# Kernel tuning notes

Hardware: AMD Instinct MI355X
Metric: run time of the kernel (lower is better)

Reference implementation:

```python
import jax, jax.numpy as jnp
import numpy as np

N, E, H, C, G = 30000, 960000, 2, 128, 64
EPS = 1e-5

def _bn(x, g, b):
    m = x.mean(0)
    v = x.var(0)  # biased, as torch BN training
    return (x - m) * jax.lax.rsqrt(v + EPS) * g + b

def setup_inputs() -> dict:
    key = jax.random.key(0)
    ks = jax.random.split(key, 16)
    s = lambda fan: 1.0 / np.sqrt(fan)
    return {
        "x": jax.random.normal(ks[0], (N, 448), jnp.float32),
        "gat_w": jax.random.normal(ks[1], (448, H * C), jnp.float32) * s(448),
        "gat_a_src": jax.random.normal(ks[2], (H, C), jnp.float32) * s(C),
        "gat_a_dst": jax.random.normal(ks[3], (H, C), jnp.float32) * s(C),
        "gat_bias": jnp.zeros((H * C,), jnp.float32),
        "mlp_w": jax.random.normal(ks[4], (H * C, 128), jnp.float32) * s(H * C),
        "mlp_b": jnp.zeros((128,), jnp.float32),
        "bn0_g": jnp.ones((128,), jnp.float32), "bn0_b": jnp.zeros((128,), jnp.float32),
        "fc1_w": jax.random.normal(ks[5], (128, 512), jnp.float32) * s(128),
        "fc1_b": jnp.zeros((512,), jnp.float32),
        "bn1_g": jnp.ones((512,), jnp.float32), "bn1_b": jnp.zeros((512,), jnp.float32),
        "fc2_w": jax.random.normal(ks[6], (512, 256), jnp.float32) * s(512),
        "fc2_b": jnp.zeros((256,), jnp.float32),
        "bn2_g": jnp.ones((256,), jnp.float32), "bn2_b": jnp.zeros((256,), jnp.float32),
        "fc3_w": jax.random.normal(ks[7], (256, 1), jnp.float32) * s(256),
        "fc3_b": jnp.zeros((1,), jnp.float32),
        "bn3_g": jnp.ones((1,), jnp.float32), "bn3_b": jnp.zeros((1,), jnp.float32),
        "edge_index": jax.random.randint(ks[8], (2, E), 0, N, jnp.int32),
        "batch": jnp.sort(jax.random.randint(ks[9], (N,), 0, G, jnp.int32)),
    }

def reference(x, gat_w, gat_a_src, gat_a_dst, gat_bias, mlp_w, mlp_b,
              bn0_g, bn0_b, fc1_w, fc1_b, bn1_g, bn1_b, fc2_w, fc2_b,
              bn2_g, bn2_b, fc3_w, fc3_b, bn3_g, bn3_b, edge_index, batch):
    # --- GATConv (eval-mode dropout = identity), self-loops added per PyG default ---
    xp = (x @ gat_w).reshape(N, H, C)                       # [N,H,C]
    a_s = (xp * gat_a_src).sum(-1)                          # [N,H]
    a_d = (xp * gat_a_dst).sum(-1)                          # [N,H]
    loops = jnp.arange(N, dtype=edge_index.dtype)
    src = jnp.concatenate([edge_index[0], loops])
    dst = jnp.concatenate([edge_index[1], loops])
    e = jax.nn.leaky_relu(a_s[src] + a_d[dst], 0.2)         # [E+N,H]
    m = jax.ops.segment_max(e, dst, num_segments=N)
    e = jnp.exp(e - m[dst])
    denom = jax.ops.segment_sum(e, dst, num_segments=N)
    alpha = e / denom[dst]                                  # softmax over in-edges
    out = jax.ops.segment_sum(alpha[:, :, None] * xp[src], dst, num_segments=N)
    out = out.reshape(N, H * C) + gat_bias                  # [N, H*C]
    # --- Scatter mlp: ELU -> (Dropout id) -> Linear -> BN ---
    h = _bn(jax.nn.elu(out) @ mlp_w + mlp_b, bn0_g, bn0_b)  # [N,128]
    # --- global_add_pool ---
    hp = jax.ops.segment_sum(h, batch, num_segments=G)      # [G,128]
    # --- fc stack: (Linear,BN,ReLU,Dropout) x2, then Linear+BN ---
    z = jax.nn.relu(_bn(hp @ fc1_w + fc1_b, bn1_g, bn1_b))
    z = jax.nn.relu(_bn(z @ fc2_w + fc2_b, bn2_g, bn2_b))
    z = _bn(z @ fc3_w + fc3_b, bn3_g, bn3_b)
    return z.reshape(-1)  # num_classes == 1
```

## Files before the change

kernel.cpp:

```cpp
#include <hip/hip_runtime.h>

#define N_NODES 30000
#define N_EDGES 960000
#define NGRAPH  64
#define BN_EPS  1e-5f
#define NBUCKET 118
#define BCAP    10240
#define GC_STRIDE 16

typedef __bf16 bf16x8 __attribute__((ext_vector_type(8)));
typedef float  f32x4  __attribute__((ext_vector_type(4)));

__device__ __forceinline__ unsigned short f2bf(float f) {
  union { float f; unsigned u; } v; v.f = f;
  unsigned r = (v.u + 0x7FFFu + ((v.u >> 16) & 1u)) >> 16;
  return (unsigned short)r;
}
__device__ __forceinline__ float bf2f(unsigned short u) {
  union { unsigned u; float f; } v; v.u = ((unsigned)u) << 16;
  return v.f;
}
__device__ __forceinline__ float bflo(unsigned w) {
  union { unsigned u; float f; } v; v.u = w << 16; return v.f;
}
__device__ __forceinline__ float bfhi(unsigned w) {
  union { unsigned u; float f; } v; v.u = w & 0xFFFF0000u; return v.f;
}
__device__ __forceinline__ void gld_lds16(const void* g, void* l) {
  __builtin_amdgcn_global_load_lds(
      (const __attribute__((address_space(1))) unsigned int*)g,
      (__attribute__((address_space(3))) unsigned int*)l, 16, 0, 0);
}

__global__ void prep_kernel(const int* __restrict__ ei,
                            int2* __restrict__ binbuf, int* __restrict__ gcur,
                            const float* __restrict__ gw, const float* __restrict__ mw,
                            unsigned short* __restrict__ wth,
                            unsigned short* __restrict__ mwth, unsigned short* __restrict__ mwtl,
                            const int* __restrict__ batch, int* __restrict__ cnt) {
  int b = blockIdx.x;
  int tid = threadIdx.x;
  if (b < 938) {
    __shared__ int lcnt[NBUCKET], lbase[NBUCKET], lcur[NBUCKET];
    int i = b * 1024 + tid * 4;
    bool val = i < N_EDGES;
    int4 dv = {0, 0, 0, 0}, sv = {0, 0, 0, 0};
    if (val) {
      dv = *(const int4*)(ei + N_EDGES + i);
      sv = *(const int4*)(ei + i);
    }
    if (tid < NBUCKET) lcnt[tid] = 0;
    __syncthreads();
    int bk0 = dv.x >> 8, bk1 = dv.y >> 8, bk2 = dv.z >> 8, bk3 = dv.w >> 8;
    if (val) {
      atomicAdd(&lcnt[bk0], 1); atomicAdd(&lcnt[bk1], 1);
      atomicAdd(&lcnt[bk2], 1); atomicAdd(&lcnt[bk3], 1);
    }
    __syncthreads();
    if (tid < NBUCKET) {
      int c = lcnt[tid];
      lbase[tid] = c ? atomicAdd(&gcur[tid * GC_STRIDE], c) : 0;
      lcur[tid] = 0;
    }
    __syncthreads();
    if (val) {
      int s0 = atomicAdd(&lcur[bk0], 1);
      binbuf[(size_t)bk0 * BCAP + lbase[bk0] + s0] = make_int2(sv.x, dv.x);
      int s1 = atomicAdd(&lcur[bk1], 1);
      binbuf[(size_t)bk1 * BCAP + lbase[bk1] + s1] = make_int2(sv.y, dv.y);
      int s2 = atomicAdd(&lcur[bk2], 1);
      binbuf[(size_t)bk2 * BCAP + lbase[bk2] + s2] = make_int2(sv.z, dv.z);
      int s3 = atomicAdd(&lcur[bk3], 1);
      binbuf[(size_t)bk3 * BCAP + lbase[bk3] + s3] = make_int2(sv.w, dv.w);
    }
    return;
  }
  if (b == 974) {
    if (tid < 64) {
      int g = tid;
      int lo = 0, hi = N_NODES;
      while (lo < hi) { int mid = (lo + hi) >> 1; if (batch[mid] < g) lo = mid + 1; else hi = mid; }
      int start = lo;
      lo = 0; hi = N_NODES;
      while (lo < hi) { int mid = (lo + hi) >> 1; if (batch[mid] < g + 1) lo = mid + 1; else hi = mid; }
      cnt[g] = lo - start;
    }
    return;
  }
  __shared__ float T[64][65];
  int b2 = b - 938;
  const float* src; unsigned short *dh, *dl; int K, Nn, kt, nt;
  if (b2 < 28) { src = gw; dh = wth; dl = nullptr; K = 448; Nn = 256; kt = b2 >> 2; nt = b2 & 3; }
  else { int b3 = b2 - 28; src = mw; dh = mwth; dl = mwtl; K = 256; Nn = 128; kt = b3 >> 1; nt = b3 & 1; }
  int nl = tid & 63, kg = tid >> 6;
#pragma unroll
  for (int j = 0; j < 16; ++j) {
    int k = kt * 64 + kg * 16 + j;
    T[kg * 16 + j][nl] = src[(size_t)k * Nn + nt * 64 + nl];
  }
  __syncthreads();
#pragma unroll
  for (int j = 0; j < 16; ++j) {
    int n = nt * 64 + kg * 16 + j;
    float v = T[nl][kg * 16 + j];
    unsigned short h = f2bf(v);
    size_t o = (size_t)n * K + kt * 64 + nl;
    dh[o] = h;
    if (dl) dl[o] = f2bf(v - bf2f(h));
  }
}

__global__ void __launch_bounds__(256) build_kernel(
    const int2* __restrict__ binbuf, const int* __restrict__ gcur,
    int* __restrict__ offs, int* __restrict__ csr) {
  __shared__ int csrL[BCAP];
  __shared__ int lcnt[256], lofs[256];
  __shared__ int wsum[4], wpre[4];
  __shared__ int redsum;
  int b = blockIdx.x, tid = threadIdx.x;
  int wv = tid >> 6, lane = tid & 63;
  int n0 = b * 256;
  int ecnt = gcur[b * GC_STRIDE];
  if (tid == 0) redsum = 0;
  lcnt[tid] = 0;
  __syncthreads();
  {
    int v = (tid < b) ? gcur[tid * GC_STRIDE] : 0;
#pragma unroll
    for (int o = 32; o; o >>= 1) v += __shfl_xor(v, o);
    if (lane == 0) atomicAdd(&redsum, v);
  }
  __syncthreads();
  int cbase = redsum;
  const int2* bp = binbuf + (size_t)b * BCAP;
  for (int e = tid; e < ecnt; e += 256) atomicAdd(&lcnt[bp[e].y - n0], 1);
  __syncthreads();
  int c = lcnt[tid];
  int s = c;
#pragma unroll
  for (int o = 1; o <= 32; o <<= 1) {
    int t = __shfl_up(s, o, 64);
    if (lane >= o) s += t;
  }
  if (lane == 63) wsum[wv] = s;
  __syncthreads();
  if (tid == 0) {
    int a = 0;
#pragma unroll
    for (int j = 0; j < 4; ++j) { wpre[j] = a; a += wsum[j]; }
  }
  __syncthreads();
  int excl = wpre[wv] + s - c;
  lofs[tid] = excl;
  int node = n0 + tid;
  if (node < N_NODES) offs[node] = cbase + excl;
  if (b == NBUCKET - 1 && tid == 0) offs[N_NODES] = cbase + ecnt;
  lcnt[tid] = 0;
  __syncthreads();
  for (int e = tid; e < ecnt; e += 256) {
    int2 p = bp[e];
    int li = p.y - n0;
    int pos = lofs[li] + atomicAdd(&lcnt[li], 1);
    csrL[pos] = p.x;
  }
  __syncthreads();
  for (int e = tid; e < ecnt; e += 256) csr[cbase + e] = csrL[e];
}

__global__ void __launch_bounds__(256) gat_gemm_kernel(
    const float* __restrict__ x,
    const unsigned short* __restrict__ wth,
    const float* __restrict__ asrc, const float* __restrict__ adst,
    unsigned short* __restrict__ xp, float* __restrict__ a_s, float* __restrict__ a_d) {
  __shared__ unsigned short Bh[4 * 128 * 8];
  int tid = threadIdx.x;
  int w = tid >> 6, lane = tid & 63;
  int m = lane & 15, quad = lane >> 4;
  int rt = blockIdx.x >> 1, ch = blockIdx.x & 1;
  int r0 = rt * 64;
  int arow = r0 + w * 16 + m;
  int arc = min(arow, N_NODES - 1);
  const float* ap = x + (size_t)arc * 448 + quad * 8;
  const unsigned short* bsh = wth + (size_t)(ch * 128) * 448;

  f32x4 acc[8];
#pragma unroll
  for (int c = 0; c < 8; ++c) acc[c] = (f32x4){0.f, 0.f, 0.f, 0.f};

  for (int kc = 0; kc < 14; ++kc) {
    int k0 = kc * 32;
#pragma unroll
    for (int i = 0; i < 2; ++i)
      gld_lds16(bsh + (size_t)(i * 64 + lane) * 448 + k0 + w * 8, Bh + w * 1024 + i * 512);
    float av[8];
    *(float4*)(av) = *(const float4*)(ap + k0);
    *(float4*)(av + 4) = *(const float4*)(ap + k0 + 4);
    bf16x8 ah, al;
#pragma unroll
    for (int j = 0; j < 8; ++j) {
      unsigned short h = f2bf(av[j]);
      unsigned short l = f2bf(av[j] - bf2f(h));
      ah[j] = *(__bf16*)&h;
      al[j] = *(__bf16*)&l;
    }
    __syncthreads();
#pragma unroll
    for (int c = 0; c < 8; ++c) {
      bf16x8 bh = *(const bf16x8*)(Bh + quad * 1024 + (c * 16 + m) * 8);
      acc[c] = __builtin_amdgcn_mfma_f32_16x16x32_bf16(ah, bh, acc[c], 0, 0, 0);
      acc[c] = __builtin_amdgcn_mfma_f32_16x16x32_bf16(al, bh, acc[c], 0, 0, 0);
    }
    __syncthreads();
  }
  float ps[4] = {0, 0, 0, 0}, pd[4] = {0, 0, 0, 0};
#pragma unroll
  for (int c = 0; c < 8; ++c) {
    int col = ch * 128 + c * 16 + m;
    float sa = asrc[col], da = adst[col];
#pragma unroll
    for (int r = 0; r < 4; ++r) {
      float v = acc[c][r];
      ps[r] += v * sa; pd[r] += v * da;
    }
  }
#pragma unroll
  for (int o = 1; o <= 8; o <<= 1) {
#pragma unroll
    for (int r = 0; r < 4; ++r) {
      ps[r] += __shfl_xor(ps[r], o);
      pd[r] += __shfl_xor(pd[r], o);
    }
  }
  int rowb = r0 + w * 16 + quad * 4;
  if (m == 0) {
#pragma unroll
    for (int r = 0; r < 4; ++r) {
      int row = rowb + r;
      if (row < N_NODES) {
        a_s[2 * row + ch] = ps[r];
        a_d[2 * row + ch] = pd[r];
      }
    }
  }
#pragma unroll
  for (int r = 0; r < 4; ++r) {
    int row = rowb + r;
    if (row < N_NODES) {
#pragma unroll
      for (int c = 0; c < 8; ++c)
        xp[(size_t)row * 256 + ch * 128 + c * 16 + m] = f2bf(acc[c][r]);
    }
  }
}

__global__ void attn_kernel(const unsigned short* __restrict__ xp,
                            const float* __restrict__ a_s, const float* __restrict__ a_d,
                            const int* __restrict__ offs, const int* __restrict__ csr,
                            const float* __restrict__ bias, unsigned short* __restrict__ y) {
  int nid = (blockIdx.x * 256 + (int)threadIdx.x) >> 6;
  int lane = threadIdx.x & 63;
  int l32 = lane & 31;
  int grp = lane >> 5;
  int h2 = l32 >> 4;
  float d0 = a_d[2 * nid], d1 = a_d[2 * nid + 1];
  float s0 = a_s[2 * nid], s1 = a_s[2 * nid + 1];
  int beg = offs[nid], end = offs[nid + 1];
  int deg = end - beg;
  float e0s = s0 + d0; e0s = e0s > 0.f ? e0s : 0.2f * e0s;
  float e1s = s1 + d1; e1s = e1s > 0.f ? e1s : 0.2f * e1s;

  if (deg <= 64) {
    int sreg = nid;
    float p0 = 0.f, p1 = 0.f;
    float e0 = -1e30f, e1 = -1e30f;
    if (lane < deg) {
      sreg = csr[beg + lane];
      float as0 = a_s[2 * sreg], as1 = a_s[2 * sreg + 1];
      e0 = as0 + d0; e0 = e0 > 0.f ? e0 : 0.2f * e0;
      e1 = as1 + d1; e1 = e1 > 0.f ? e1 : 0.2f * e1;
    }
    float m0 = fmaxf(e0, e0s), m1 = fmaxf(e1, e1s);
#pragma unroll
    for (int o = 32; o; o >>= 1) {
      m0 = fmaxf(m0, __shfl_xor(m0, o));
      m1 = fmaxf(m1, __shfl_xor(m1, o));
    }
    if (lane < deg) { p0 = __expf(e0 - m0); p1 = __expf(e1 - m1); }
    float ws0 = p0, ws1 = p1;
#pragma unroll
    for (int o = 32; o; o >>= 1) { ws0 += __shfl_xor(ws0, o); ws1 += __shfl_xor(ws1, o); }
    float wself0 = __expf(e0s - m0), wself1 = __expf(e1s - m1);
    float inv = 1.f / (h2 ? (ws1 + wself1) : (ws0 + wself0));

    float acc[8] = {0.f, 0.f, 0.f, 0.f, 0.f, 0.f, 0.f, 0.f};
    const unsigned* xpw = (const unsigned*)xp;
    {
      float wgt = grp ? 0.f : (h2 ? wself1 : wself0);
      uint4 u = *(const uint4*)(xpw + (size_t)nid * 128 + l32 * 4);
      acc[0] += wgt * bflo(u.x); acc[1] += wgt * bfhi(u.x);
      acc[2] += wgt * bflo(u.y); acc[3] += wgt * bfhi(u.y);
      acc[4] += wgt * bflo(u.z); acc[5] += wgt * bfhi(u.z);
      acc[6] += wgt * bflo(u.w); acc[7] += wgt * bfhi(u.w);
    }
    for (int j0 = 0; j0 < deg; j0 += 16) {
      int si[8]; float g[8];
#pragma unroll
      for (int i = 0; i < 8; ++i) {
        int e = j0 + 2 * i + grp;
        si[i] = __shfl(sreg, e);
        float a0 = __shfl(p0, e), a1 = __shfl(p1, e);
        g[i] = h2 ? a1 : a0;
      }
      uint4 u[8];
#pragma unroll
      for (int i = 0; i < 8; ++i)
        u[i] = *(const uint4*)(xpw + (size_t)si[i] * 128 + l32 * 4);
#pragma unroll
      for (int i = 0; i < 8; ++i) {
        acc[0] += g[i] * bflo(u[i].x); acc[1] += g[i] * bfhi(u[i].x);
        acc[2] += g[i] * bflo(u[i].y); acc[3] += g[i] * bfhi(u[i].y);
        acc[4] += g[i] * bflo(u[i].z); acc[5] += g[i] * bfhi(u[i].z);
        acc[6] += g[i] * bflo(u[i].w); acc[7] += g[i] * bfhi(u[i].w);
      }
    }
#pragma unroll
    for (int i = 0; i < 8; ++i) acc[i] += __shfl_xor(acc[i], 32);
    if (grp == 0) {
      int c0 = l32 * 8;
      float4 b0 = *(const float4*)(bias + c0);
      float4 b1 = *(const float4*)(bias + c0 + 4);
      float ob[8] = {b0.x, b0.y, b0.z, b0.w, b1.x, b1.y, b1.z, b1.w};
      unsigned short h[8];
#pragma unroll
      for (int i = 0; i < 8; ++i) {
        float v = acc[i] * inv + ob[i];
        v = v > 0.f ? v : __expf(v) - 1.f;
        h[i] = f2bf(v);
      }
      uint4 o;
      o.x = (unsigned)h[0] | ((unsigned)h[1] << 16);
      o.y = (unsigned)h[2] | ((unsigned)h[3] << 16);
      o.z = (unsigned)h[4] | ((unsigned)h[5] << 16);
      o.w = (unsigned)h[6] | ((unsigned)h[7] << 16);
      *(uint4*)(y + (size_t)nid * 256 + c0) = o;
    }
    return;
  }

  int head = lane >> 5;
  float m0 = e0s, m1 = e1s;
  for (int j = beg + lane; j < end; j += 64) {
    int s = csr[j];
    float as0 = a_s[2 * s], as1 = a_s[2 * s + 1];
    float e0 = as0 + d0; e0 = e0 > 0.f ? e0 : 0.2f * e0;
    float e1 = as1 + d1; e1 = e1 > 0.f ? e1 : 0.2f * e1;
    m0 = fmaxf(m0, e0); m1 = fmaxf(m1, e1);
  }
#pragma unroll
  for (int o = 32; o; o >>= 1) {
    m0 = fmaxf(m0, __shfl_xor(m0, o));
    m1 = fmaxf(m1, __shfl_xor(m1, o));
  }
  float dh = head ? d1 : d0;
  float mh = head ? m1 : m0;
  float ax, ay, az, aw, wsum;
  {
    float e = head ? e1s : e0s;
    float wgt = __expf(e - mh);
    ushort4 u = *(const ushort4*)(xp + (size_t)nid * 256 + lane * 4);
    ax = wgt * bf2f(u.x); ay = wgt * bf2f(u.y); az = wgt * bf2f(u.z); aw = wgt * bf2f(u.w);
    wsum = wgt;
  }
  for (int j = beg; j < end; ++j) {
    int s = csr[j];
    float as = a_s[2 * s + head];
    float e = as + dh; e = e > 0.f ? e : 0.2f * e;
    float wgt = __expf(e - mh);
    ushort4 u = *(const ushort4*)(xp + (size_t)s * 256 + lane * 4);
    ax += wgt * bf2f(u.x); ay += wgt * bf2f(u.y); az += wgt * bf2f(u.z); aw += wgt * bf2f(u.w);
    wsum += wgt;
  }
  float inv = 1.f / wsum;
  float4 b4 = *(const float4*)(bias + lane * 4);
  float o0 = ax * inv + b4.x, o1 = ay * inv + b4.y;
  float o2 = az * inv + b4.z, o3 = aw * inv + b4.w;
  o0 = o0 > 0.f ? o0 : __expf(o0) - 1.f;
  o1 = o1 > 0.f ? o1 : __expf(o1) - 1.f;
  o2 = o2 > 0.f ? o2 : __expf(o2) - 1.f;
  o3 = o3 > 0.f ? o3 : __expf(o3) - 1.f;
  ushort4 yo; yo.x = f2bf(o0); yo.y = f2bf(o1); yo.z = f2bf(o2); yo.w = f2bf(o3);
  *(ushort4*)(y + (size_t)nid * 256 + lane * 4) = yo;
}

__global__ void __launch_bounds__(256) mlp_gemm_kernel(
    const unsigned short* __restrict__ y,
    const unsigned short* __restrict__ mwth, const unsigned short* __restrict__ mwtl,
    const float* __restrict__ mlp_b, const int* __restrict__ batch,
    float* __restrict__ S, float* __restrict__ Q) {
  __shared__ unsigned short Bh[4 * 128 * 8], Bl[4 * 128 * 8];
  __shared__ float Sloc[128], Qloc[128];
  int tid = threadIdx.x;
  int w = tid >> 6, lane = tid & 63;
  int m = lane & 15, quad = lane >> 4;
  int r0 = blockIdx.x * 64;
  if (tid < 128) { Sloc[tid] = 0.f; Qloc[tid] = 0.f; }
  const unsigned short* ap = y + (size_t)(r0 + w * 16 + m) * 256 + quad * 8;

  f32x4 acc[8];
#pragma unroll
  for (int c = 0; c < 8; ++c) acc[c] = (f32x4){0.f, 0.f, 0.f, 0.f};

  for (int kc = 0; kc < 8; ++kc) {
    int k0 = kc * 32;
#pragma unroll
    for (int i = 0; i < 2; ++i) {
      int n = i * 64 + lane;
      gld_lds16(mwth + (size_t)n * 256 + k0 + w * 8, Bh + w * 1024 + i * 512);
      gld_lds16(mwtl + (size_t)n * 256 + k0 + w * 8, Bl + w * 1024 + i * 512);
    }
    bf16x8 ah = *(const bf16x8*)(ap + k0);
    __syncthreads();
#pragma unroll
    for (int c = 0; c < 8; ++c) {
      bf16x8 bh = *(const bf16x8*)(Bh + quad * 1024 + (c * 16 + m) * 8);
      bf16x8 bl = *(const bf16x8*)(Bl + quad * 1024 + (c * 16 + m) * 8);
      acc[c] = __builtin_amdgcn_mfma_f32_16x16x32_bf16(ah, bh, acc[c], 0, 0, 0);
      acc[c] = __builtin_amdgcn_mfma_f32_16x16x32_bf16(ah, bl, acc[c], 0, 0, 0);
    }
    __syncthreads();
  }
  int rowb = r0 + w * 16 + quad * 4;
  int gfirst = batch[r0];
  int glast = batch[min(r0 + 63, N_NODES - 1)];
  bool uni = (gfirst == glast);
  bool valid[4]; int gg[4];
#pragma unroll
  for (int r = 0; r < 4; ++r) {
    int row = rowb + r;
    valid[r] = row < N_NODES;
    gg[r] = (!uni && valid[r]) ? batch[row] : gfirst;
  }
#pragma unroll
  for (int c = 0; c < 8; ++c) {
    int col = c * 16 + m;
    float bv = mlp_b[col];
    float sc = 0.f, qc = 0.f;
#pragma unroll
    for (int r = 0; r < 4; ++r) {
      if (valid[r]) {
        float v = acc[c][r] + bv;
        qc += v * v;
        if (uni) sc += v;
        else atomicAdd(&S[gg[r] * 128 + col], v);
      }
    }
    qc += __shfl_xor(qc, 16); qc += __shfl_xor(qc, 32);
    sc += __shfl_xor(sc, 16); sc += __shfl_xor(sc, 32);
    if (quad == 0) {
      atomicAdd(&Qloc[col], qc);
      if (uni) atomicAdd(&Sloc[col], sc);
    }
  }
  __syncthreads();
  if (tid < 128) {
    atomicAdd(&Q[tid], Qloc[tid]);
    if (uni) atomicAdd(&S[gfirst * 128 + tid], Sloc[tid]);
  }
}

__global__ void fc1_kernel(const float* __restrict__ S, const float* __restrict__ Q,
                           const int* __restrict__ cnt, const float* __restrict__ g0,
                           const float* __restrict__ b0,
                           const float* __restrict__ w, const float* __restrict__ b,
                           const float* __restrict__ bng, const float* __restrict__ bnb,
                           float* __restrict__ z1t) {
  __shared__ float hp[64 * 129];
  int tid = threadIdx.x;
  if (tid < 128) {
    int c = tid;
    float sum = 0.f;
    for (int g = 0; g < NGRAPH; ++g) sum += S[g * 128 + c];
    float mu = sum / (float)N_NODES;
    float var = Q[c] / (float)N_NODES - mu * mu;
    float gam = g0[c] * rsqrtf(var + BN_EPS);
    float bet = b0[c];
    for (int g = 0; g < NGRAPH; ++g) {
      float k = (float)cnt[g];
      hp[g * 129 + c] = gam * (S[g * 128 + c] - k * mu) + k * bet;
    }
  }
  __syncthreads();
  int wv = tid >> 6, lane = tid & 63;
  int j = blockIdx.x * 4 + wv;
  float acc = b[j];
  for (int c = 0; c < 128; ++c) acc += hp[lane * 129 + c] * w[c * 512 + j];
  float s1 = acc, s2 = acc * acc;
#pragma unroll
  for (int o = 32; o; o >>= 1) { s1 += __shfl_xor(s1, o); s2 += __shfl_xor(s2, o); }
  float mu = s1 * (1.f / 64.f), var = s2 * (1.f / 64.f) - mu * mu;
  float z = bng[j] * (acc - mu) * rsqrtf(var + BN_EPS) + bnb[j];
  z1t[j * 64 + lane] = fmaxf(z, 0.f);
}

__global__ void fc2_kernel(const float* __restrict__ z1t, const float* __restrict__ w,
                           const float* __restrict__ b, const float* __restrict__ bng,
                           const float* __restrict__ bnb, float* __restrict__ z2t) {
  int wv = threadIdx.x >> 6, lane = threadIdx.x & 63;
  int j = blockIdx.x * 4 + wv;
  float acc = b[j];
  for (int c = 0; c < 512; ++c) acc += z1t[c * 64 + lane] * w[c * 256 + j];
  float s1 = acc, s2 = acc * acc;
#pragma unroll
  for (int o = 32; o; o >>= 1) { s1 += __shfl_xor(s1, o); s2 += __shfl_xor(s2, o); }
  float mu = s1 * (1.f / 64.f), var = s2 * (1.f / 64.f) - mu * mu;
  float z = bng[j] * (acc - mu) * rsqrtf(var + BN_EPS) + bnb[j];
  z2t[j * 64 + lane] = fmaxf(z, 0.f);
}

__global__ void fc3_kernel(const float* __restrict__ z2t, const float* __restrict__ w,
                           const float* __restrict__ b, const float* __restrict__ bng,
                           const float* __restrict__ bnb, float* __restrict__ out) {
  int lane = threadIdx.x;
  float acc = b[0];
  for (int c = 0; c < 256; ++c) acc += z2t[c * 64 + lane] * w[c];
  float s1 = acc, s2 = acc * acc;
#pragma unroll
  for (int o = 32; o; o >>= 1) { s1 += __shfl_xor(s1, o); s2 += __shfl_xor(s2, o); }
  float mu = s1 * (1.f / 64.f), var = s2 * (1.f / 64.f) - mu * mu;
  out[lane] = bng[0] * (acc - mu) * rsqrtf(var + BN_EPS) + bnb[0];
}

extern "C" void kernel_launch(void* const* d_in, const int* in_sizes, int n_in,
                              void* d_out, int out_size, void* d_ws, size_t ws_size,
                              hipStream_t stream) {
  const float* x     = (const float*)d_in[0];
  const float* gat_w = (const float*)d_in[1];
  const float* a_src = (const float*)d_in[2];
  const float* a_dst = (const float*)d_in[3];
  const float* gbias = (const float*)d_in[4];
  const float* mlp_w = (const float*)d_in[5];
  const float* mlp_b = (const float*)d_in[6];
  const float* bn0g  = (const float*)d_in[7];
  const float* bn0b  = (const float*)d_in[8];
  const float* fc1w  = (const float*)d_in[9];
  const float* fc1b  = (const float*)d_in[10];
  const float* bn1g  = (const float*)d_in[11];
  const float* bn1b  = (const float*)d_in[12];
  const float* fc2w  = (const float*)d_in[13];
  const float* fc2b  = (const float*)d_in[14];
  const float* bn2g  = (const float*)d_in[15];
  const float* bn2b  = (const float*)d_in[16];
  const float* fc3w  = (const float*)d_in[17];
  const float* fc3b  = (const float*)d_in[18];
  const float* bn3g  = (const float*)d_in[19];
  const float* bn3b  = (const float*)d_in[20];
  const int* eidx    = (const int*)d_in[21];
  const int* batch   = (const int*)d_in[22];
  float* out = (float*)d_out;

  char* base = (char*)d_ws;
  size_t off = 0;
  auto take = [&](size_t bytes) -> char* {
    char* p = base + off;
    off += (bytes + 255) & ~(size_t)255;
    return p;
  };
  unsigned short* xp   = (unsigned short*)take((size_t)N_NODES * 256 * 2);
  unsigned short* ybf  = (unsigned short*)take((size_t)30016 * 256 * 2);
  unsigned short* wth  = (unsigned short*)take(448 * 256 * 2);
  unsigned short* mwth = (unsigned short*)take(128 * 256 * 2);
  unsigned short* mwtl = (unsigned short*)take(128 * 256 * 2);
  float* a_s = (float*)take((size_t)N_NODES * 2 * 4);
  float* a_d = (float*)take((size_t)N_NODES * 2 * 4);
  int* offs  = (int*)take((size_t)(N_NODES + 1) * 4);
  int* csr   = (int*)take((size_t)N_EDGES * 4);
  int2* binbuf = (int2*)take((size_t)NBUCKET * BCAP * 8);
  int* gcur  = (int*)take((size_t)NBUCKET * GC_STRIDE * 4);
  float* S   = (float*)take(NGRAPH * 128 * 4);
  float* Q   = (float*)take(128 * 4);
  int* cnt   = (int*)take(NGRAPH * 4);
  float* z1t = (float*)take(512 * 64 * 4);
  float* z2t = (float*)take(256 * 64 * 4);

  hipMemsetAsync(gcur, 0, (size_t)NBUCKET * GC_STRIDE * 4, stream);
  hipMemsetAsync(S, 0, (size_t)(NGRAPH * 128 * 4 + 512), stream);

  prep_kernel<<<975, 256, 0, stream>>>(eidx, binbuf, gcur, gat_w, mlp_w,
                                       wth, mwth, mwtl, batch, cnt);
  build_kernel<<<NBUCKET, 256, 0, stream>>>(binbuf, gcur, offs, csr);
  gat_gemm_kernel<<<938, 256, 0, stream>>>(x, wth, a_src, a_dst, xp, a_s, a_d);
  attn_kernel<<<7500, 256, 0, stream>>>(xp, a_s, a_d, offs, csr, gbias, ybf);
  mlp_gemm_kernel<<<469, 256, 0, stream>>>(ybf, mwth, mwtl, mlp_b, batch, S, Q);
  fc1_kernel<<<128, 256, 0, stream>>>(S, Q, cnt, bn0g, bn0b, fc1w, fc1b, bn1g, bn1b, z1t);
  fc2_kernel<<<64, 256, 0, stream>>>(z1t, fc2w, fc2b, bn2g, bn2b, z2t);
  fc3_kernel<<<1, 64, 0, stream>>>(z2t, fc3w, fc3b, bn3g, bn3b, out);

  (void)in_sizes; (void)n_in; (void)out_size; (void)ws_size;
}
```

Measured before the change: 361.4 us.

## Fuse CSR build with GAT GEMM, double-buffer GEMMs, stage binning in LDS

The CSR build kernel and the GAT projection GEMM are merged into one launch, with the first blocks doing the build and the rest the GEMM, so the two overlap and one launch is saved. Both GEMMs now double-buffer their B tiles and A loads to hide global latency, and xp is written through LDS as coalesced 16-byte stores. The MLP GEMM is split over two column halves, doubling the block count. Edge binning in prep is staged through LDS so the global writes are grouped by bucket. BCAP is lowered to 8960, which risks overflowing a bucket if one receives more edges than that.

New measurement: 334.3 us. -7.5%, faster.

```diff
diff --git a/kernel.cpp b/kernel.cpp
--- a/kernel.cpp
+++ b/kernel.cpp
@@ -5,8 +5,9 @@
 #define NGRAPH  64
 #define BN_EPS  1e-5f
 #define NBUCKET 118
-#define BCAP    10240
+#define BCAP    8960
 #define GC_STRIDE 16
+#define BLD_N   118
 
 typedef __bf16 bf16x8 __attribute__((ext_vector_type(8)));
 typedef float  f32x4  __attribute__((ext_vector_type(4)));
@@ -41,7 +42,8 @@
   int b = blockIdx.x;
   int tid = threadIdx.x;
   if (b < 938) {
-    __shared__ int lcnt[NBUCKET], lbase[NBUCKET], lcur[NBUCKET];
+    __shared__ int lcnt[NBUCKET], lofs[NBUCKET], lbase[NBUCKET];
+    __shared__ int2 ebuf[1024];
     int i = b * 1024 + tid * 4;
     bool val = i < N_EDGES;
     int4 dv = {0, 0, 0, 0}, sv = {0, 0, 0, 0};
@@ -57,21 +59,29 @@
       atomicAdd(&lcnt[bk2], 1); atomicAdd(&lcnt[bk3], 1);
     }
     __syncthreads();
+    if (tid == 0) {
+      int run = 0;
+      for (int j = 0; j < NBUCKET; ++j) { lofs[j] = run; run += lcnt[j]; }
+    }
+    __syncthreads();
     if (tid < NBUCKET) {
       int c = lcnt[tid];
       lbase[tid] = c ? atomicAdd(&gcur[tid * GC_STRIDE], c) : 0;
-      lcur[tid] = 0;
+      lcnt[tid] = 0;
     }
     __syncthreads();
     if (val) {
-      int s0 = atomicAdd(&lcur[bk0], 1);
-      binbuf[(size_t)bk0 * BCAP + lbase[bk0] + s0] = make_int2(sv.x, dv.x);
-      int s1 = atomicAdd(&lcur[bk1], 1);
-      binbuf[(size_t)bk1 * BCAP + lbase[bk1] + s1] = make_int2(sv.y, dv.y);
-      int s2 = atomicAdd(&lcur[bk2], 1);
-      binbuf[(size_t)bk2 * BCAP + lbase[bk2] + s2] = make_int2(sv.z, dv.z);
-      int s3 = atomicAdd(&lcur[bk3], 1);
-      binbuf[(size_t)bk3 * BCAP + lbase[bk3] + s3] = make_int2(sv.w, dv.w);
+      int s0 = atomicAdd(&lcnt[bk0], 1); ebuf[lofs[bk0] + s0] = make_int2(sv.x, dv.x);
+      int s1 = atomicAdd(&lcnt[bk1], 1); ebuf[lofs[bk1] + s1] = make_int2(sv.y, dv.y);
+      int s2 = atomicAdd(&lcnt[bk2], 1); ebuf[lofs[bk2] + s2] = make_int2(sv.z, dv.z);
+      int s3 = atomicAdd(&lcnt[bk3], 1); ebuf[lofs[bk3] + s3] = make_int2(sv.w, dv.w);
+    }
+    __syncthreads();
+    int tot = min(1024, N_EDGES - b * 1024);
+    for (int e = tid; e < tot; e += 256) {
+      int2 p = ebuf[e];
+      int bk = p.y >> 8;
+      binbuf[(size_t)bk * BCAP + lbase[bk] + (e - lofs[bk])] = p;
     }
     return;
   }
@@ -110,91 +120,106 @@
   }
 }
 
-__global__ void __launch_bounds__(256) build_kernel(
+__global__ void __launch_bounds__(256) gat_build_kernel(
     const int2* __restrict__ binbuf, const int* __restrict__ gcur,
-    int* __restrict__ offs, int* __restrict__ csr) {
-  __shared__ int csrL[BCAP];
-  __shared__ int lcnt[256], lofs[256];
-  __shared__ int wsum[4], wpre[4];
-  __shared__ int redsum;
-  int b = blockIdx.x, tid = threadIdx.x;
-  int wv = tid >> 6, lane = tid & 63;
-  int n0 = b * 256;
-  int ecnt = gcur[b * GC_STRIDE];
-  if (tid == 0) redsum = 0;
-  lcnt[tid] = 0;
-  __syncthreads();
-  {
-    int v = (tid < b) ? gcur[tid * GC_STRIDE] : 0;
-#pragma unroll
-    for (int o = 32; o; o >>= 1) v += __shfl_xor(v, o);
-    if (lane == 0) atomicAdd(&redsum, v);
-  }
-  __syncthreads();
-  int cbase = redsum;
-  const int2* bp = binbuf + (size_t)b * BCAP;
-  for (int e = tid; e < ecnt; e += 256) atomicAdd(&lcnt[bp[e].y - n0], 1);
-  __syncthreads();
-  int c = lcnt[tid];
-  int s = c;
-#pragma unroll
-  for (int o = 1; o <= 32; o <<= 1) {
-    int t = __shfl_up(s, o, 64);
-    if (lane >= o) s += t;
-  }
-  if (lane == 63) wsum[wv] = s;
-  __syncthreads();
-  if (tid == 0) {
-    int a = 0;
-#pragma unroll
-    for (int j = 0; j < 4; ++j) { wpre[j] = a; a += wsum[j]; }
-  }
-  __syncthreads();
-  int excl = wpre[wv] + s - c;
-  lofs[tid] = excl;
-  int node = n0 + tid;
-  if (node < N_NODES) offs[node] = cbase + excl;
-  if (b == NBUCKET - 1 && tid == 0) offs[N_NODES] = cbase + ecnt;
-  lcnt[tid] = 0;
-  __syncthreads();
-  for (int e = tid; e < ecnt; e += 256) {
-    int2 p = bp[e];
-    int li = p.y - n0;
-    int pos = lofs[li] + atomicAdd(&lcnt[li], 1);
-    csrL[pos] = p.x;
-  }
-  __syncthreads();
-  for (int e = tid; e < ecnt; e += 256) csr[cbase + e] = csrL[e];
-}
-
-__global__ void __launch_bounds__(256) gat_gemm_kernel(
-    const float* __restrict__ x,
-    const unsigned short* __restrict__ wth,
+    int* __restrict__ offs, int* __restrict__ csr,
+    const float* __restrict__ x, const unsigned short* __restrict__ wth,
     const float* __restrict__ asrc, const float* __restrict__ adst,
     unsigned short* __restrict__ xp, float* __restrict__ a_s, float* __restrict__ a_d) {
-  __shared__ unsigned short Bh[4 * 128 * 8];
+  __shared__ __align__(16) int smemI[9728];
   int tid = threadIdx.x;
-  int w = tid >> 6, lane = tid & 63;
+  int wv = tid >> 6, lane = tid & 63;
+  if (blockIdx.x < BLD_N) {
+    int* csrL = smemI;
+    int* lcnt = smemI + 8960;
+    int* lofs = smemI + 9216;
+    int* wsum = smemI + 9472;
+    int* wpre = smemI + 9476;
+    int* redsum = smemI + 9480;
+    int b = blockIdx.x;
+    int n0 = b * 256;
+    int ecnt = gcur[b * GC_STRIDE];
+    if (tid == 0) *redsum = 0;
+    lcnt[tid] = 0;
+    __syncthreads();
+    {
+      int v = (tid < b) ? gcur[tid * GC_STRIDE] : 0;
+#pragma unroll
+      for (int o = 32; o; o >>= 1) v += __shfl_xor(v, o);
+      if (lane == 0) atomicAdd(redsum, v);
+    }
+    __syncthreads();
+    int cbase = *redsum;
+    const int2* bp = binbuf + (size_t)b * BCAP;
+    for (int e = tid; e < ecnt; e += 256) atomicAdd(&lcnt[bp[e].y - n0], 1);
+    __syncthreads();
+    int c = lcnt[tid];
+    int s = c;
+#pragma unroll
+    for (int o = 1; o <= 32; o <<= 1) {
+      int t = __shfl_up(s, o, 64);
+      if (lane >= o) s += t;
+    }
+    if (lane == 63) wsum[wv] = s;
+    __syncthreads();
+    if (tid == 0) {
+      int a = 0;
+#pragma unroll
+      for (int j = 0; j < 4; ++j) { wpre[j] = a; a += wsum[j]; }
+    }
+    __syncthreads();
+    int excl = wpre[wv] + s - c;
+    lofs[tid] = excl;
+    int node = n0 + tid;
+    if (node < N_NODES) offs[node] = cbase + excl;
+    if (b == BLD_N - 1 && tid == 0) offs[N_NODES] = cbase + ecnt;
+    lcnt[tid] = 0;
+    __syncthreads();
+    for (int e = tid; e < ecnt; e += 256) {
+      int2 p = bp[e];
+      int li = p.y - n0;
+      int pos = lofs[li] + atomicAdd(&lcnt[li], 1);
+      csrL[pos] = p.x;
+    }
+    __syncthreads();
+    for (int e = tid; e < ecnt; e += 256) csr[cbase + e] = csrL[e];
+    return;
+  }
+  int t = (int)blockIdx.x - BLD_N;
   int m = lane & 15, quad = lane >> 4;
-  int rt = blockIdx.x >> 1, ch = blockIdx.x & 1;
+  int rt = t >> 1, ch = t & 1;
   int r0 = rt * 64;
-  int arow = r0 + w * 16 + m;
+  int arow = r0 + wv * 16 + m;
   int arc = min(arow, N_NODES - 1);
   const float* ap = x + (size_t)arc * 448 + quad * 8;
   const unsigned short* bsh = wth + (size_t)(ch * 128) * 448;
+  unsigned short* B0 = (unsigned short*)smemI;
+  unsigned short* B1 = B0 + 4096;
 
   f32x4 acc[8];
 #pragma unroll
   for (int c = 0; c < 8; ++c) acc[c] = (f32x4){0.f, 0.f, 0.f, 0.f};
 
+  float4 v0 = *(const float4*)(ap);
+  float4 v1 = *(const float4*)(ap + 4);
+#pragma unroll
+  for (int i = 0; i < 2; ++i)
+    gld_lds16(bsh + (size_t)(i * 64 + lane) * 448 + wv * 8, B0 + wv * 1024 + i * 512);
+
   for (int kc = 0; kc < 14; ++kc) {
-    int k0 = kc * 32;
-#pragma unroll
-    for (int i = 0; i < 2; ++i)
-      gld_lds16(bsh + (size_t)(i * 64 + lane) * 448 + k0 + w * 8, Bh + w * 1024 + i * 512);
-    float av[8];
-    *(float4*)(av) = *(const float4*)(ap + k0);
-    *(float4*)(av + 4) = *(const float4*)(ap + k0 + 4);
+    unsigned short* Bc = (kc & 1) ? B1 : B0;
+    unsigned short* Bn = (kc & 1) ? B0 : B1;
+    __syncthreads();
+    float4 p0, p1;
+    if (kc < 13) {
+      int k0n = (kc + 1) * 32;
+#pragma unroll
+      for (int i = 0; i < 2; ++i)
+        gld_lds16(bsh + (size_t)(i * 64 + lane) * 448 + k0n + wv * 8, Bn + wv * 1024 + i * 512);
+      p0 = *(const float4*)(ap + k0n);
+      p1 = *(const float4*)(ap + k0n + 4);
+    }
+    float av[8] = {v0.x, v0.y, v0.z, v0.w, v1.x, v1.y, v1.z, v1.w};
     bf16x8 ah, al;
 #pragma unroll
     for (int j = 0; j < 8; ++j) {
@@ -203,14 +228,13 @@
       ah[j] = *(__bf16*)&h;
       al[j] = *(__bf16*)&l;
     }
-    __syncthreads();
 #pragma unroll
     for (int c = 0; c < 8; ++c) {
-      bf16x8 bh = *(const bf16x8*)(Bh + quad * 1024 + (c * 16 + m) * 8);
+      bf16x8 bh = *(const bf16x8*)(Bc + quad * 1024 + (c * 16 + m) * 8);
       acc[c] = __builtin_amdgcn_mfma_f32_16x16x32_bf16(ah, bh, acc[c], 0, 0, 0);
       acc[c] = __builtin_amdgcn_mfma_f32_16x16x32_bf16(al, bh, acc[c], 0, 0, 0);
     }
-    __syncthreads();
+    if (kc < 13) { v0 = p0; v1 = p1; }
   }
   float ps[4] = {0, 0, 0, 0}, pd[4] = {0, 0, 0, 0};
 #pragma unroll
@@ -231,7 +255,7 @@
       pd[r] += __shfl_xor(pd[r], o);
     }
   }
-  int rowb = r0 + w * 16 + quad * 4;
+  int rowb = r0 + wv * 16 + quad * 4;
   if (m == 0) {
 #pragma unroll
     for (int r = 0; r < 4; ++r) {
@@ -242,14 +266,20 @@
       }
     }
   }
-#pragma unroll
-  for (int r = 0; r < 4; ++r) {
-    int row = rowb + r;
-    if (row < N_NODES) {
-#pragma unroll
-      for (int c = 0; c < 8; ++c)
-        xp[(size_t)row * 256 + ch * 128 + c * 16 + m] = f2bf(acc[c][r]);
-    }
+  __syncthreads();
+  unsigned short* st = (unsigned short*)smemI + wv * 2048;
+#pragma unroll
+  for (int c = 0; c < 8; ++c)
+#pragma unroll
+    for (int r = 0; r < 4; ++r)
+      st[(quad * 4 + r) * 128 + c * 16 + m] = f2bf(acc[c][r]);
+#pragma unroll
+  for (int p = 0; p < 4; ++p) {
+    int rl = p * 4 + quad;
+    uint4 vv = *(const uint4*)(st + rl * 128 + m * 8);
+    int row = r0 + wv * 16 + rl;
+    if (row < N_NODES)
+      *(uint4*)(xp + (size_t)row * 256 + ch * 128 + m * 8) = vv;
   }
 }
 
@@ -397,37 +427,45 @@
     const unsigned short* __restrict__ mwth, const unsigned short* __restrict__ mwtl,
     const float* __restrict__ mlp_b, const int* __restrict__ batch,
     float* __restrict__ S, float* __restrict__ Q) {
-  __shared__ unsigned short Bh[4 * 128 * 8], Bl[4 * 128 * 8];
-  __shared__ float Sloc[128], Qloc[128];
+  __shared__ unsigned short Bh[2][2048], Bl[2][2048];
+  __shared__ float Sloc[64], Qloc[64];
   int tid = threadIdx.x;
   int w = tid >> 6, lane = tid & 63;
   int m = lane & 15, quad = lane >> 4;
-  int r0 = blockIdx.x * 64;
-  if (tid < 128) { Sloc[tid] = 0.f; Qloc[tid] = 0.f; }
+  int rb = blockIdx.x >> 1, ch = blockIdx.x & 1;
+  int r0 = rb * 64;
+  if (tid < 64) { Sloc[tid] = 0.f; Qloc[tid] = 0.f; }
   const unsigned short* ap = y + (size_t)(r0 + w * 16 + m) * 256 + quad * 8;
-
-  f32x4 acc[8];
-#pragma unroll
-  for (int c = 0; c < 8; ++c) acc[c] = (f32x4){0.f, 0.f, 0.f, 0.f};
+  const unsigned short* bh = mwth + (size_t)(ch * 64) * 256;
+  const unsigned short* bl = mwtl + (size_t)(ch * 64) * 256;
+
+  f32x4 acc[4];
+#pragma unroll
+  for (int c = 0; c < 4; ++c) acc[c] = (f32x4){0.f, 0.f, 0.f, 0.f};
+
+  bf16x8 a_cur = *(const bf16x8*)(ap);
+  gld_lds16(bh + (size_t)lane * 256 + w * 8, &Bh[0][w * 512]);
+  gld_lds16(bl + (size_t)lane * 256 + w * 8, &Bl[0][w * 512]);
 
   for (int kc = 0; kc < 8; ++kc) {
-    int k0 = kc * 32;
-#pragma unroll
-    for (int i = 0; i < 2; ++i) {
-      int n = i * 64 + lane;
-      gld_lds16(mwth + (size_t)n * 256 + k0 + w * 8, Bh + w * 1024 + i * 512);
-      gld_lds16(mwtl + (size_t)n * 256 + k0 + w * 8, Bl + w * 1024 + i * 512);
-    }
-    bf16x8 ah = *(const bf16x8*)(ap + k0);
-    __syncthreads();
-#pragma unroll
-    for (int c = 0; c < 8; ++c) {
-      bf16x8 bh = *(const bf16x8*)(Bh + quad * 1024 + (c * 16 + m) * 8);
-      bf16x8 bl = *(const bf16x8*)(Bl + quad * 1024 + (c * 16 + m) * 8);
-      acc[c] = __builtin_amdgcn_mfma_f32_16x16x32_bf16(ah, bh, acc[c], 0, 0, 0);
-      acc[c] = __builtin_amdgcn_mfma_f32_16x16x32_bf16(ah, bl, acc[c], 0, 0, 0);
-    }
-    __syncthreads();
+    const unsigned short* Bch = Bh[kc & 1];
+    const unsigned short* Bcl = Bl[kc & 1];
+    __syncthreads();
+    bf16x8 a_nxt = a_cur;
+    if (kc < 7) {
+      int k0n = (kc + 1) * 32;
+      gld_lds16(bh + (size_t)lane * 256 + k0n + w * 8, &Bh[(kc + 1) & 1][w * 512]);
+      gld_lds16(bl + (size_t)lane * 256 + k0n + w * 8, &Bl[(kc + 1) & 1][w * 512]);
+      a_nxt = *(const bf16x8*)(ap + k0n);
+    }
+#pragma unroll
+    for (int c = 0; c < 4; ++c) {
+      bf16x8 vh = *(const bf16x8*)(Bch + quad * 512 + (c * 16 + m) * 8);
+      bf16x8 vl = *(const bf16x8*)(Bcl + quad * 512 + (c * 16 + m) * 8);
+      acc[c] = __builtin_amdgcn_mfma_f32_16x16x32_bf16(a_cur, vh, acc[c], 0, 0, 0);
+      acc[c] = __builtin_amdgcn_mfma_f32_16x16x32_bf16(a_cur, vl, acc[c], 0, 0, 0);
+    }
+    a_cur = a_nxt;
   }
   int rowb = r0 + w * 16 + quad * 4;
   int gfirst = batch[r0];
@@ -441,8 +479,9 @@
     gg[r] = (!uni && valid[r]) ? batch[row] : gfirst;
   }
 #pragma unroll
-  for (int c = 0; c < 8; ++c) {
-    int col = c * 16 + m;
+  for (int c = 0; c < 4; ++c) {
+    int cl = c * 16 + m;
+    int col = ch * 64 + cl;
     float bv = mlp_b[col];
     float sc = 0.f, qc = 0.f;
 #pragma unroll
@@ -457,14 +496,14 @@
     qc += __shfl_xor(qc, 16); qc += __shfl_xor(qc, 32);
     sc += __shfl_xor(sc, 16); sc += __shfl_xor(sc, 32);
     if (quad == 0) {
-      atomicAdd(&Qloc[col], qc);
-      if (uni) atomicAdd(&Sloc[col], sc);
+      atomicAdd(&Qloc[cl], qc);
+      if (uni) atomicAdd(&Sloc[cl], sc);
     }
   }
   __syncthreads();
-  if (tid < 128) {
-    atomicAdd(&Q[tid], Qloc[tid]);
-    if (uni) atomicAdd(&S[gfirst * 128 + tid], Sloc[tid]);
+  if (tid < 64) {
+    atomicAdd(&Q[ch * 64 + tid], Qloc[tid]);
+    if (uni) atomicAdd(&S[gfirst * 128 + ch * 64 + tid], Sloc[tid]);
   }
 }
 
@@ -587,10 +626,10 @@
 
   prep_kernel<<<975, 256, 0, stream>>>(eidx, binbuf, gcur, gat_w, mlp_w,
                                        wth, mwth, mwtl, batch, cnt);
-  build_kernel<<<NBUCKET, 256, 0, stream>>>(binbuf, gcur, offs, csr);
-  gat_gemm_kernel<<<938, 256, 0, stream>>>(x, wth, a_src, a_dst, xp, a_s, a_d);
+  gat_build_kernel<<<BLD_N + 938, 256, 0, stream>>>(binbuf, gcur, offs, csr,
+                                                    x, wth, a_src, a_dst, xp, a_s, a_d);
   attn_kernel<<<7500, 256, 0, stream>>>(xp, a_s, a_d, offs, csr, gbias, ybf);
-  mlp_gemm_kernel<<<469, 256, 0, stream>>>(ybf, mwth, mwtl, mlp_b, batch, S, Q);
+  mlp_gemm_kernel<<<938, 256, 0, stream>>>(ybf, mwth, mwtl, mlp_b, batch, S, Q);
   fc1_kernel<<<128, 256, 0, stream>>>(S, Q, cnt, bn0g, bn0b, fc1w, fc1b, bn1g, bn1b, z1t);
   fc2_kernel<<<64, 256, 0, stream>>>(z1t, fc2w, fc2b, bn2g, bn2b, z2t);
   fc3_kernel<<<1, 64, 0, stream>>>(z2t, fc3w, fc3b, bn3g, bn3b, out);
```
